# Performance work log

Hardware: AMD Instinct MI355X
Metric: run time of the kernel (lower is better)

## Reference

```python
import jax, jax.numpy as jnp
import numpy as np

LN_EPS = 1e-5

def setup_inputs() -> dict:
    key = jax.random.key(0)
    ks = jax.random.split(key, 10)
    L, B, D, C, O = 512, 2, 256, 128, 64
    s_in = 1.0 / np.sqrt(D)
    s_ch = 1.0 / np.sqrt(C)
    return {
        "x": jax.random.normal(ks[0], (L, B, D), dtype=jnp.float32),
        "ln_gamma": jnp.ones((D,), dtype=jnp.float32),
        "ln_beta": jnp.zeros((D,), dtype=jnp.float32),
        "w1": jax.random.uniform(ks[1], (D, C), jnp.float32, -s_in, s_in),
        "b1": jax.random.uniform(ks[2], (C,), jnp.float32, -s_in, s_in),
        "w2": jax.random.uniform(ks[3], (D, C), jnp.float32, -s_in, s_in),
        "b2": jax.random.uniform(ks[4], (C,), jnp.float32, -s_in, s_in),
        "w3": jax.random.uniform(ks[5], (C, O), jnp.float32, -s_ch, s_ch),
        "b3": jax.random.uniform(ks[6], (O,), jnp.float32, -s_ch, s_ch),
        "w4": jax.random.uniform(ks[7], (C, O), jnp.float32, -s_ch, s_ch),
    }

def _layernorm(x, gamma, beta):
    mu = jnp.mean(x, axis=-1, keepdims=True)
    var = jnp.mean(jnp.square(x - mu), axis=-1, keepdims=True)
    return (x - mu) * jax.lax.rsqrt(var + LN_EPS) * gamma + beta

def reference(x, ln_gamma, ln_beta, w1, b1, w2, b2, w3, b3, w4):
    # x: (L, B, D) -> (B, L, D)
    xb = jnp.transpose(x, (1, 0, 2))
    xb = _layernorm(xb, ln_gamma, ln_beta)
    a = xb @ w1 + b1  # (B, L, C)
    b = xb @ w2 + b2  # (B, L, C)
    # (a_l * b_m) @ w3  -> contract channel dim directly into output channels
    mul_term = jnp.einsum('blc,bmc,co->blmo', a, b, w3) + b3
    # (a_l - b_m) @ w4  -> distribute linearity to avoid (B,L,L,C) materialization
    a4 = a @ w4  # (B, L, O)
    b4 = b @ w4  # (B, L, O)
    sub_term = a4[:, :, None, :] - b4[:, None, :, :]
    return mul_term + sub_term  # (B, L, L, O)
```

## Files before the change

### kernel.cpp

```cpp
#include <hip/hip_runtime.h>
#include <hip/hip_bf16.h>

#define LL 512
#define BB 2
#define DD 256
#define CC 128
#define OO 64

#define WT_STRIDE 136

typedef __attribute__((ext_vector_type(8))) short bf16x8;
typedef __attribute__((ext_vector_type(4))) float f32x4;

__device__ __forceinline__ short f2bf(float v) {
    __hip_bfloat16 h = __float2bfloat16(v);
    return *reinterpret_cast<short*>(&h);
}

__device__ __forceinline__ float wave_reduce_sum(float v) {
#pragma unroll
    for (int off = 32; off > 0; off >>= 1)
        v += __shfl_down(v, off, 64);
    return v;
}

__global__ __launch_bounds__(256) void prep_kernel(
    const float* __restrict__ x,
    const float* __restrict__ gamma,
    const float* __restrict__ beta,
    const float* __restrict__ w1, const float* __restrict__ b1,
    const float* __restrict__ w2, const float* __restrict__ b2,
    const float* __restrict__ w4, const float* __restrict__ b3,
    float* __restrict__ a_ws, __hip_bfloat16* __restrict__ bact,
    float* __restrict__ a4b3_ws, float* __restrict__ b4_ws)
{
    const int blk = blockIdx.x;
    const int b = blk >> 9;
    const int l = blk & (LL - 1);
    const int t = threadIdx.x;

    __shared__ float ylds[DD];
    __shared__ float ab[2 * CC];
    __shared__ float red[8];

    float xv = x[(l * BB + b) * DD + t];
    float s = wave_reduce_sum(xv);
    if ((t & 63) == 0) red[t >> 6] = s;
    __syncthreads();
    float mu = (red[0] + red[1] + red[2] + red[3]) * (1.0f / DD);
    float xc = xv - mu;
    float s2 = wave_reduce_sum(xc * xc);
    if ((t & 63) == 0) red[4 + (t >> 6)] = s2;
    __syncthreads();
    float var = (red[4] + red[5] + red[6] + red[7]) * (1.0f / DD);
    float y = xc * rsqrtf(var + 1e-5f) * gamma[t] + beta[t];
    ylds[t] = y;
    __syncthreads();

    {
        const int c = t & (CC - 1);
        const float* w = (t < CC) ? w1 : w2;
        float acc = (t < CC) ? b1[c] : b2[c];
#pragma unroll 16
        for (int d = 0; d < DD; ++d)
            acc = fmaf(ylds[d], w[d * CC + c], acc);
        ab[t] = acc;
        if (t < CC) {
            a_ws[(b * LL + l) * CC + c] = acc;
        } else {
            bact[(b * LL + l) * CC + c] = __float2bfloat16(acc);
        }
    }
    __syncthreads();

    if (t < 2 * OO) {
        const int o = t & (OO - 1);
        const float* src = (t < OO) ? ab : (ab + CC);
        float acc = (t < OO) ? b3[o] : 0.0f;
#pragma unroll 16
        for (int c = 0; c < CC; ++c)
            acc = fmaf(src[c], w4[c * OO + o], acc);
        float* dst = (t < OO) ? a4b3_ws : b4_ws;
        dst[(b * LL + l) * OO + o] = acc;
    }
}

__global__ __launch_bounds__(256, 3) void main_kernel(
    const float* __restrict__ a_ws, const __hip_bfloat16* __restrict__ bact,
    const float* __restrict__ a4b3_ws, const float* __restrict__ b4_ws,
    const float* __restrict__ w3,
    float* __restrict__ out)
{
    const int bid = blockIdx.x;
    const int mh = bid & 1;
    const int l  = (bid >> 1) & (LL - 1);
    const int b  = bid >> 10;
    const int t  = threadIdx.x;
    const int wave = t >> 6;
    const int lane = t & 63;
    const int ln = lane & 15;
    const int q  = lane >> 4;

    __shared__ short Wt[OO * WT_STRIDE];

    const float* arow = a_ws + (b * LL + l) * CC;
    const float4* w3v4 = (const float4*)w3;
#pragma unroll
    for (int i4 = t; i4 < CC * OO / 4; i4 += 256) {
        const int c = i4 >> 4;
        const int o = (i4 & 15) * 4;
        const float ac = arow[c];
        const float4 wv = w3v4[i4];
        Wt[(o + 0) * WT_STRIDE + c] = f2bf(ac * wv.x);
        Wt[(o + 1) * WT_STRIDE + c] = f2bf(ac * wv.y);
        Wt[(o + 2) * WT_STRIDE + c] = f2bf(ac * wv.z);
        Wt[(o + 3) * WT_STRIDE + c] = f2bf(ac * wv.w);
    }
    __syncthreads();

    const int mbase = mh * 256 + wave * 64;

    const short* abase = (const short*)bact + ((size_t)(b * LL + mbase + ln)) * CC + q * 8;
    const short* wbase = &Wt[ln * WT_STRIDE + q * 8];

    f32x4 acc[4][4];
#pragma unroll
    for (int mt = 0; mt < 4; ++mt)
#pragma unroll
        for (int ot = 0; ot < 4; ++ot)
            acc[mt][ot] = (f32x4){0.f, 0.f, 0.f, 0.f};

#pragma unroll
    for (int ks = 0; ks < 4; ++ks) {
        bf16x8 af[4], bfr[4];
#pragma unroll
        for (int mt = 0; mt < 4; ++mt)
            af[mt] = *(const bf16x8*)(abase + mt * (16 * CC) + ks * 32);
#pragma unroll
        for (int ot = 0; ot < 4; ++ot)
            bfr[ot] = *(const bf16x8*)(wbase + ot * (16 * WT_STRIDE) + ks * 32);
#pragma unroll
        for (int mt = 0; mt < 4; ++mt)
#pragma unroll
            for (int ot = 0; ot < 4; ++ot)
                acc[mt][ot] = __builtin_amdgcn_mfma_f32_16x16x32_bf16(
                    af[mt], bfr[ot], acc[mt][ot], 0, 0, 0);
    }

    float a4v[4];
    const float* a4p = a4b3_ws + (b * LL + l) * OO;
#pragma unroll
    for (int ot = 0; ot < 4; ++ot)
        a4v[ot] = a4p[ot * 16 + ln];

#pragma unroll
    for (int mt = 0; mt < 4; ++mt) {
        const int mrow = mbase + mt * 16 + q * 4;
        const float* b4p = b4_ws + ((size_t)(b * LL + mrow)) * OO + ln;
        float* outp = out + (((size_t)(b * LL + l)) * LL + mrow) * OO + ln;
#pragma unroll
        for (int ot = 0; ot < 4; ++ot) {
#pragma unroll
            for (int r = 0; r < 4; ++r) {
                outp[r * OO + ot * 16] = acc[mt][ot][r] + a4v[ot] - b4p[r * OO + ot * 16];
            }
        }
    }
}

extern "C" void kernel_launch(void* const* d_in, const int* in_sizes, int n_in,
                              void* d_out, int out_size, void* d_ws, size_t ws_size,
                              hipStream_t stream) {
    const float* x     = (const float*)d_in[0];
    const float* gamma = (const float*)d_in[1];
    const float* beta  = (const float*)d_in[2];
    const float* w1    = (const float*)d_in[3];
    const float* b1    = (const float*)d_in[4];
    const float* w2    = (const float*)d_in[5];
    const float* b2    = (const float*)d_in[6];
    const float* w3    = (const float*)d_in[7];
    const float* b3    = (const float*)d_in[8];
    const float* w4    = (const float*)d_in[9];
    float* out = (float*)d_out;

    char* ws = (char*)d_ws;
    float* a_ws            = (float*)ws;
    __hip_bfloat16* bact   = (__hip_bfloat16*)(ws + 512*1024);
    float* a4b3_ws         = (float*)(ws + 768*1024);
    float* b4_ws           = (float*)(ws + 1024*1024);

    prep_kernel<<<BB * LL, 256, 0, stream>>>(x, gamma, beta, w1, b1, w2, b2,
                                             w4, b3, a_ws, bact, a4b3_ws, b4_ws);
    main_kernel<<<BB * LL * 2, 256, 0, stream>>>(a_ws, bact, a4b3_ws, b4_ws,
                                                 w3, out);
}
```

Measured before the change: 187.6 us.

## Pre-swizzle w3 to bf16 fragments and drop LDS staging in main kernel

```diff
diff --git a/kernel.cpp b/kernel.cpp
--- a/kernel.cpp
+++ b/kernel.cpp
@@ -7,14 +7,17 @@
 #define CC 128
 #define OO 64
 
-#define WT_STRIDE 136
-
 typedef __attribute__((ext_vector_type(8))) short bf16x8;
 typedef __attribute__((ext_vector_type(4))) float f32x4;
 
 __device__ __forceinline__ short f2bf(float v) {
     __hip_bfloat16 h = __float2bfloat16(v);
     return *reinterpret_cast<short*>(&h);
+}
+__device__ __forceinline__ float bf2f(short s) {
+    __hip_bfloat16 h;
+    *reinterpret_cast<short*>(&h) = s;
+    return __bfloat162float(h);
 }
 
 __device__ __forceinline__ float wave_reduce_sum(float v) {
@@ -31,13 +34,29 @@
     const float* __restrict__ w1, const float* __restrict__ b1,
     const float* __restrict__ w2, const float* __restrict__ b2,
     const float* __restrict__ w4, const float* __restrict__ b3,
-    float* __restrict__ a_ws, __hip_bfloat16* __restrict__ bact,
-    float* __restrict__ a4b3_ws, float* __restrict__ b4_ws)
+    const float* __restrict__ w3,
+    float* __restrict__ a_ws, short* __restrict__ bact,
+    float* __restrict__ a4b3_ws, float* __restrict__ b4_ws,
+    short* __restrict__ w3s)
 {
     const int blk = blockIdx.x;
+    const int t = threadIdx.x;
+
+    if (blk >= BB * LL) {
+        const int e  = (blk - BB * LL) * 256 + t;
+        const int j  = e & 7;
+        const int ln = (e >> 3) & 15;
+        const int q  = (e >> 7) & 3;
+        const int ks = (e >> 9) & 3;
+        const int ot = e >> 11;
+        const int c = ks * 32 + q * 8 + j;
+        const int o = ot * 16 + ln;
+        w3s[e] = f2bf(w3[c * OO + o]);
+        return;
+    }
+
     const int b = blk >> 9;
     const int l = blk & (LL - 1);
-    const int t = threadIdx.x;
 
     __shared__ float ylds[DD];
     __shared__ float ab[2 * CC];
@@ -60,35 +79,72 @@
     {
         const int c = t & (CC - 1);
         const float* w = (t < CC) ? w1 : w2;
-        float acc = (t < CC) ? b1[c] : b2[c];
-#pragma unroll 16
-        for (int d = 0; d < DD; ++d)
-            acc = fmaf(ylds[d], w[d * CC + c], acc);
-        ab[t] = acc;
-        if (t < CC) {
-            a_ws[(b * LL + l) * CC + c] = acc;
-        } else {
-            bact[(b * LL + l) * CC + c] = __float2bfloat16(acc);
-        }
+        const float4* y4 = (const float4*)ylds;
+        float acc0 = (t < CC) ? b1[c] : b2[c];
+        float acc1 = 0.f, acc2 = 0.f, acc3 = 0.f;
+#pragma unroll
+        for (int i = 0; i < 64; i += 4) {
+            float4 ya = y4[i], yb = y4[i + 1], yc = y4[i + 2], yd = y4[i + 3];
+            const float* wp = w + i * 4 * CC + c;
+            acc0 = fmaf(ya.x, wp[0 * CC], acc0);
+            acc0 = fmaf(ya.y, wp[1 * CC], acc0);
+            acc0 = fmaf(ya.z, wp[2 * CC], acc0);
+            acc0 = fmaf(ya.w, wp[3 * CC], acc0);
+            acc1 = fmaf(yb.x, wp[4 * CC], acc1);
+            acc1 = fmaf(yb.y, wp[5 * CC], acc1);
+            acc1 = fmaf(yb.z, wp[6 * CC], acc1);
+            acc1 = fmaf(yb.w, wp[7 * CC], acc1);
+            acc2 = fmaf(yc.x, wp[8 * CC], acc2);
+            acc2 = fmaf(yc.y, wp[9 * CC], acc2);
+            acc2 = fmaf(yc.z, wp[10 * CC], acc2);
+            acc2 = fmaf(yc.w, wp[11 * CC], acc2);
+            acc3 = fmaf(yd.x, wp[12 * CC], acc3);
+            acc3 = fmaf(yd.y, wp[13 * CC], acc3);
+            acc3 = fmaf(yd.z, wp[14 * CC], acc3);
+            acc3 = fmaf(yd.w, wp[15 * CC], acc3);
+        }
+        float accv = (acc0 + acc1) + (acc2 + acc3);
+        ab[t] = accv;
+        if (t < CC) a_ws[(b * LL + l) * CC + c] = accv;
+        else        bact[(b * LL + l) * CC + c] = f2bf(accv);
     }
     __syncthreads();
 
     if (t < 2 * OO) {
         const int o = t & (OO - 1);
-        const float* src = (t < OO) ? ab : (ab + CC);
-        float acc = (t < OO) ? b3[o] : 0.0f;
-#pragma unroll 16
-        for (int c = 0; c < CC; ++c)
-            acc = fmaf(src[c], w4[c * OO + o], acc);
-        float* dst = (t < OO) ? a4b3_ws : b4_ws;
-        dst[(b * LL + l) * OO + o] = acc;
+        const float4* s4 = (const float4*)((t < OO) ? ab : (ab + CC));
+        float acc0 = (t < OO) ? b3[o] : 0.0f;
+        float acc1 = 0.f, acc2 = 0.f, acc3 = 0.f;
+#pragma unroll
+        for (int i = 0; i < 32; i += 4) {
+            float4 sa = s4[i], sb = s4[i + 1], sc = s4[i + 2], sd = s4[i + 3];
+            const float* wp = w4 + i * 4 * OO + o;
+            acc0 = fmaf(sa.x, wp[0 * OO], acc0);
+            acc0 = fmaf(sa.y, wp[1 * OO], acc0);
+            acc0 = fmaf(sa.z, wp[2 * OO], acc0);
+            acc0 = fmaf(sa.w, wp[3 * OO], acc0);
+            acc1 = fmaf(sb.x, wp[4 * OO], acc1);
+            acc1 = fmaf(sb.y, wp[5 * OO], acc1);
+            acc1 = fmaf(sb.z, wp[6 * OO], acc1);
+            acc1 = fmaf(sb.w, wp[7 * OO], acc1);
+            acc2 = fmaf(sc.x, wp[8 * OO], acc2);
+            acc2 = fmaf(sc.y, wp[9 * OO], acc2);
+            acc2 = fmaf(sc.z, wp[10 * OO], acc2);
+            acc2 = fmaf(sc.w, wp[11 * OO], acc2);
+            acc3 = fmaf(sd.x, wp[12 * OO], acc3);
+            acc3 = fmaf(sd.y, wp[13 * OO], acc3);
+            acc3 = fmaf(sd.z, wp[14 * OO], acc3);
+            acc3 = fmaf(sd.w, wp[15 * OO], acc3);
+        }
+        float accv = (acc0 + acc1) + (acc2 + acc3);
+        ((t < OO) ? a4b3_ws : b4_ws)[(b * LL + l) * OO + o] = accv;
     }
 }
 
 __global__ __launch_bounds__(256, 3) void main_kernel(
-    const float* __restrict__ a_ws, const __hip_bfloat16* __restrict__ bact,
+    const float* __restrict__ a_ws, const short* __restrict__ bact,
     const float* __restrict__ a4b3_ws, const float* __restrict__ b4_ws,
-    const float* __restrict__ w3,
+    const short* __restrict__ w3s,
     float* __restrict__ out)
 {
     const int bid = blockIdx.x;
@@ -100,70 +156,70 @@
     const int lane = t & 63;
     const int ln = lane & 15;
     const int q  = lane >> 4;
-
-    __shared__ short Wt[OO * WT_STRIDE];
+    const int mbase = mh * 256 + wave * 64;
 
     const float* arow = a_ws + (b * LL + l) * CC;
-    const float4* w3v4 = (const float4*)w3;
-#pragma unroll
-    for (int i4 = t; i4 < CC * OO / 4; i4 += 256) {
-        const int c = i4 >> 4;
-        const int o = (i4 & 15) * 4;
-        const float ac = arow[c];
-        const float4 wv = w3v4[i4];
-        Wt[(o + 0) * WT_STRIDE + c] = f2bf(ac * wv.x);
-        Wt[(o + 1) * WT_STRIDE + c] = f2bf(ac * wv.y);
-        Wt[(o + 2) * WT_STRIDE + c] = f2bf(ac * wv.z);
-        Wt[(o + 3) * WT_STRIDE + c] = f2bf(ac * wv.w);
-    }
-    __syncthreads();
-
-    const int mbase = mh * 256 + wave * 64;
-
-    const short* abase = (const short*)bact + ((size_t)(b * LL + mbase + ln)) * CC + q * 8;
-    const short* wbase = &Wt[ln * WT_STRIDE + q * 8];
+    const short* abase = bact + (size_t)(b * LL + mbase + ln) * CC + q * 8;
 
     f32x4 acc[4][4];
 #pragma unroll
-    for (int mt = 0; mt < 4; ++mt)
+    for (int ot = 0; ot < 4; ++ot)
+#pragma unroll
+        for (int mt = 0; mt < 4; ++mt)
+            acc[ot][mt] = (f32x4){0.f, 0.f, 0.f, 0.f};
+
+#pragma unroll
+    for (int ks = 0; ks < 4; ++ks) {
+        const float* ap = arow + ks * 32 + q * 8;
+        float av[8];
+        *(float4*)&av[0] = *(const float4*)ap;
+        *(float4*)&av[4] = *(const float4*)(ap + 4);
+
+        bf16x8 wp[4];
+#pragma unroll
+        for (int ot = 0; ot < 4; ++ot) {
+            bf16x8 wr = *(const bf16x8*)(w3s + (((ot * 4 + ks) * 4 + q) << 7) + ln * 8);
+            bf16x8 r;
+#pragma unroll
+            for (int j = 0; j < 8; ++j)
+                r[j] = f2bf(bf2f(wr[j]) * av[j]);
+            wp[ot] = r;
+        }
+
+        bf16x8 bfr[4];
+#pragma unroll
+        for (int mt = 0; mt < 4; ++mt)
+            bfr[mt] = *(const bf16x8*)(abase + mt * 16 * CC + ks * 32);
+
 #pragma unroll
         for (int ot = 0; ot < 4; ++ot)
-            acc[mt][ot] = (f32x4){0.f, 0.f, 0.f, 0.f};
-
-#pragma unroll
-    for (int ks = 0; ks < 4; ++ks) {
-        bf16x8 af[4], bfr[4];
-#pragma unroll
-        for (int mt = 0; mt < 4; ++mt)
-            af[mt] = *(const bf16x8*)(abase + mt * (16 * CC) + ks * 32);
-#pragma unroll
-        for (int ot = 0; ot < 4; ++ot)
-            bfr[ot] = *(const bf16x8*)(wbase + ot * (16 * WT_STRIDE) + ks * 32);
-#pragma unroll
-        for (int mt = 0; mt < 4; ++mt)
-#pragma unroll
-            for (int ot = 0; ot < 4; ++ot)
-                acc[mt][ot] = __builtin_amdgcn_mfma_f32_16x16x32_bf16(
-                    af[mt], bfr[ot], acc[mt][ot], 0, 0, 0);
-    }
-
-    float a4v[4];
+#pragma unroll
+            for (int mt = 0; mt < 4; ++mt)
+                acc[ot][mt] = __builtin_amdgcn_mfma_f32_16x16x32_bf16(
+                    wp[ot], bfr[mt], acc[ot][mt], 0, 0, 0);
+    }
+
     const float* a4p = a4b3_ws + (b * LL + l) * OO;
+    float4 a4v[4];
 #pragma unroll
     for (int ot = 0; ot < 4; ++ot)
-        a4v[ot] = a4p[ot * 16 + ln];
+        a4v[ot] = *(const float4*)(a4p + ot * 16 + q * 4);
 
 #pragma unroll
     for (int mt = 0; mt < 4; ++mt) {
-        const int mrow = mbase + mt * 16 + q * 4;
-        const float* b4p = b4_ws + ((size_t)(b * LL + mrow)) * OO + ln;
-        float* outp = out + (((size_t)(b * LL + l)) * LL + mrow) * OO + ln;
+        const int m = mbase + mt * 16 + ln;
+        const float* b4p = b4_ws + (size_t)(b * LL + m) * OO;
+        float* op = out + ((size_t)(b * LL + l) * LL + m) * OO;
 #pragma unroll
         for (int ot = 0; ot < 4; ++ot) {
-#pragma unroll
-            for (int r = 0; r < 4; ++r) {
-                outp[r * OO + ot * 16] = acc[mt][ot][r] + a4v[ot] - b4p[r * OO + ot * 16];
-            }
+            float4 bq = *(const float4*)(b4p + ot * 16 + q * 4);
+            f32x4 a = acc[ot][mt];
+            float4 r;
+            r.x = a[0] + a4v[ot].x - bq.x;
+            r.y = a[1] + a4v[ot].y - bq.y;
+            r.z = a[2] + a4v[ot].z - bq.z;
+            r.w = a[3] + a4v[ot].w - bq.w;
+            *(float4*)(op + ot * 16 + q * 4) = r;
         }
     }
 }
@@ -184,13 +240,15 @@
     float* out = (float*)d_out;
 
     char* ws = (char*)d_ws;
-    float* a_ws            = (float*)ws;
-    __hip_bfloat16* bact   = (__hip_bfloat16*)(ws + 512*1024);
-    float* a4b3_ws         = (float*)(ws + 768*1024);
-    float* b4_ws           = (float*)(ws + 1024*1024);
-
-    prep_kernel<<<BB * LL, 256, 0, stream>>>(x, gamma, beta, w1, b1, w2, b2,
-                                             w4, b3, a_ws, bact, a4b3_ws, b4_ws);
+    float* a_ws    = (float*)ws;
+    short* bact    = (short*)(ws + 512 * 1024);
+    float* a4b3_ws = (float*)(ws + 768 * 1024);
+    float* b4_ws   = (float*)(ws + 1024 * 1024);
+    short* w3s     = (short*)(ws + 1280 * 1024);
+
+    prep_kernel<<<BB * LL + 32, 256, 0, stream>>>(x, gamma, beta, w1, b1, w2, b2,
+                                                  w4, b3, w3,
+                                                  a_ws, bact, a4b3_ws, b4_ws, w3s);
     main_kernel<<<BB * LL * 2, 256, 0, stream>>>(a_ws, bact, a4b3_ws, b4_ws,
-                                                 w3, out);
-}
+                                                 w3s, out);
+}
```

Result: slower. 194.2 us (+3.5%).
